# Kernel optimization log

Hardware: AMD Instinct MI355X
Metric: run time of the kernel (lower is better)

## Reference

```python
import jax, jax.numpy as jnp
import numpy as np

N = 100000
E = 1200000
D = 64
OUT_A = 2
OUT_B = 21


def setup_inputs() -> dict:
    key = jax.random.key(0)
    ks = jax.random.split(key, 12)
    v = jax.random.normal(ks[0], (N, D), dtype=jnp.float32)
    edge_src = jax.random.randint(ks[1], (E,), 0, N, dtype=jnp.int32)
    edge_dst = jax.random.randint(ks[2], (E,), 0, N, dtype=jnp.int32)
    rel_type = jax.random.randint(ks[3], (E,), 0, 3, dtype=jnp.int32)
    norm = jax.random.uniform(ks[4], (E,), dtype=jnp.float32)
    # relation weights per layer, kaiming-uniform-ish scale
    bound = float(np.sqrt(6.0 / D))
    W1 = jax.random.uniform(ks[5], (3, D, D), dtype=jnp.float32, minval=-bound, maxval=bound)
    W2 = jax.random.uniform(ks[6], (3, D, D), dtype=jnp.float32, minval=-bound, maxval=bound)
    W3 = jax.random.uniform(ks[7], (3, D, D), dtype=jnp.float32, minval=-bound, maxval=bound)
    Wa = jax.random.uniform(ks[8], (OUT_A, D), dtype=jnp.float32, minval=-bound, maxval=bound)
    ba = jnp.zeros((OUT_A,), dtype=jnp.float32)
    Wb = jax.random.uniform(ks[9], (OUT_B, D), dtype=jnp.float32, minval=-bound, maxval=bound)
    bb = jnp.zeros((OUT_B,), dtype=jnp.float32)
    return {"v": v, "edge_src": edge_src, "edge_dst": edge_dst, "rel_type": rel_type,
            "norm": norm, "W1": W1, "W2": W2, "W3": W3,
            "Wa": Wa, "ba": ba, "Wb": Wb, "bb": bb}


def _rgcn_layer(x, W, edge_src, edge_dst, rel_type, norm, skip):
    # Transform all nodes by each of the 3 relation matrices (cheap: 3 small GEMMs),
    # then gather per-edge: equivalent to bmm(h_src[e], W[rel_type[e]]).
    hr = jnp.einsum('nd,rde->rne', x, W)            # [3, N, D]
    msg = hr[rel_type, edge_src] * norm[:, None]     # [E, D]
    agg = jax.ops.segment_sum(msg, edge_dst, num_segments=x.shape[0])  # [N, D]
    return jax.nn.relu(agg + x) if skip else jax.nn.relu(agg)


def reference(v, edge_src, edge_dst, rel_type, norm, W1, W2, W3, Wa, ba, Wb, bb):
    x = _rgcn_layer(v, W1, edge_src, edge_dst, rel_type, norm, skip=False)
    x = _rgcn_layer(x, W2, edge_src, edge_dst, rel_type, norm, skip=True)
    x = _rgcn_layer(x, W3, edge_src, edge_dst, rel_type, norm, skip=True)
    xa = x @ Wa.T + ba
    xb = x @ Wb.T + bb
    return (xa, xb)
```

## Files before the change

kernel.cpp:

```cpp
#include <hip/hip_runtime.h>

#define D 64
#define NREL 3
#define SRC_MASK 0x1FFFF
#define ATHR 512
#define APT 8
#define ABLK (ATHR * APT)
#define BSH 9
#define BSZ 512

typedef unsigned short bf16_t;
typedef __attribute__((ext_vector_type(8))) short short8v;
typedef __attribute__((ext_vector_type(4))) float float4v;

__device__ __forceinline__ float bf2f(unsigned int u16) {
  return __uint_as_float(u16 << 16);
}
__device__ __forceinline__ unsigned int f2bf(float f) {
  unsigned int x = __float_as_uint(f);
  return (x + 0x7fffu + ((x >> 16) & 1u)) >> 16;
}

__global__ __launch_bounds__(512) void zero_kernel(int* __restrict__ a,
                                                   int* __restrict__ b, int n) {
  const int t = threadIdx.x;
  for (int i = t; i < n; i += 512) { a[i] = 0; b[i] = 0; }
}

__global__ __launch_bounds__(256) void conv_kernel(
    const float* __restrict__ in, bf16_t* __restrict__ out, int n4) {
  const int i = blockIdx.x * 256 + threadIdx.x;
  if (i >= n4) return;
  const float4 f = reinterpret_cast<const float4*>(in)[i];
  uint2 o;
  o.x = f2bf(f.x) | (f2bf(f.y) << 16);
  o.y = f2bf(f.z) | (f2bf(f.w) << 16);
  reinterpret_cast<uint2*>(out)[i] = o;
}

__global__ __launch_bounds__(256) void transform_kernel(
    const bf16_t* __restrict__ xb, const float* __restrict__ W,
    bf16_t* __restrict__ hr, int n_nodes) {
  __shared__ bf16_t wt[NREL * 64 * 72];
  const int tid = threadIdx.x;

  for (int idx = tid; idx < NREL * 64 * 64; idx += 256) {
    const int r = idx >> 12;
    const int k = (idx >> 6) & 63;
    const int od = idx & 63;
    wt[(r * 64 + od) * 72 + k] = (bf16_t)f2bf(W[idx]);
  }
  __syncthreads();

  const int wid = tid >> 6;
  const int lane = tid & 63;
  const int n0 = blockIdx.x * 64 + wid * 16;
  if (n0 >= n_nodes) return;

  const bf16_t* xrow = &xb[(long)(n0 + (lane & 15)) * 64 + (lane >> 4) * 8];
  const short8v bx0 = *reinterpret_cast<const short8v*>(xrow);
  const short8v bx1 = *reinterpret_cast<const short8v*>(xrow + 32);

  const int node = n0 + (lane & 15);
#pragma unroll
  for (int r = 0; r < NREL; ++r) {
#pragma unroll
    for (int t = 0; t < 4; ++t) {
      const bf16_t* wrow =
          &wt[(r * 64 + t * 16 + (lane & 15)) * 72 + (lane >> 4) * 8];
      const short8v a0 = *reinterpret_cast<const short8v*>(wrow);
      const short8v a1 = *reinterpret_cast<const short8v*>(wrow + 32);
      float4v acc = {0.f, 0.f, 0.f, 0.f};
      acc = __builtin_amdgcn_mfma_f32_16x16x32_bf16(a0, bx0, acc, 0, 0, 0);
      acc = __builtin_amdgcn_mfma_f32_16x16x32_bf16(a1, bx1, acc, 0, 0, 0);
      const int od = t * 16 + (lane >> 4) * 4;
      uint2 o;
      o.x = f2bf(acc[0]) | (f2bf(acc[1]) << 16);
      o.y = f2bf(acc[2]) | (f2bf(acc[3]) << 16);
      *reinterpret_cast<uint2*>(&hr[((long)r * n_nodes + node) * 64 + od]) = o;
    }
  }
}

__global__ __launch_bounds__(ATHR) void bhist_kernel(
    const int* __restrict__ dst, int* __restrict__ bdeg, int n_edges, int nb) {
  __shared__ int cnt[200];
  const int t = threadIdx.x;
  for (int b = t; b < nb; b += ATHR) cnt[b] = 0;
  __syncthreads();
  const long e0 = (long)blockIdx.x * ABLK;
#pragma unroll
  for (int i = 0; i < APT; ++i) {
    const long e = e0 + t + (long)i * ATHR;
    if (e < n_edges) atomicAdd(&cnt[dst[e] >> BSH], 1);
  }
  __syncthreads();
  for (int b = t; b < nb; b += ATHR)
    if (cnt[b]) atomicAdd(&bdeg[b], cnt[b]);
}

__global__ __launch_bounds__(512) void bscan_kernel(
    const int* __restrict__ bdeg, int* __restrict__ boffs, int nb) {
  __shared__ int s[512];
  const int t = threadIdx.x;
  const int v = (t < nb) ? bdeg[t] : 0;
  s[t] = v;
  __syncthreads();
  for (int off = 1; off < 512; off <<= 1) {
    const int add = (t >= off) ? s[t - off] : 0;
    __syncthreads();
    s[t] += add;
    __syncthreads();
  }
  if (t < nb) boffs[t] = s[t] - v;
  if (t == 511) boffs[nb] = s[nb - 1];
}

__global__ __launch_bounds__(ATHR) void binA_kernel(
    const int* __restrict__ src, const int* __restrict__ dst,
    const int* __restrict__ rel, const float* __restrict__ norm,
    const int* __restrict__ boffs, int* __restrict__ bcur,
    int2* __restrict__ binpay, int n_edges, int nb) {
  __shared__ int cnt[200];
  __shared__ int basea[200];
  const int t = threadIdx.x;
  const long e0 = (long)blockIdx.x * ABLK;

  for (int b = t; b < nb; b += ATHR) cnt[b] = 0;
  __syncthreads();

  int2 pay[APT];
  int bk[APT], slot[APT];
#pragma unroll
  for (int i = 0; i < APT; ++i) {
    const long e = e0 + t + (long)i * ATHR;
    if (e < n_edges) {
      const int d = dst[e];
      bk[i] = d >> BSH;
      pay[i] = make_int2(src[e] | (rel[e] << 17) | ((d & (BSZ - 1)) << 19),
                         __float_as_int(norm[e]));
      slot[i] = atomicAdd(&cnt[bk[i]], 1);
    } else {
      bk[i] = -1;
    }
  }
  __syncthreads();

  for (int b = t; b < nb; b += ATHR) {
    const int c = cnt[b];
    basea[b] = c ? (boffs[b] + atomicAdd(&bcur[b], c)) : 0;
  }
  __syncthreads();

#pragma unroll
  for (int i = 0; i < APT; ++i) {
    if (bk[i] >= 0) binpay[basea[bk[i]] + slot[i]] = pay[i];
  }
}

__global__ __launch_bounds__(512) void binB_kernel(
    const int2* __restrict__ binpay, const int* __restrict__ boffs,
    int2* __restrict__ edgebuf, int* __restrict__ deg, int* __restrict__ offs,
    int n_nodes) {
  __shared__ int cnt[512];
  __shared__ int ss[512];
  __shared__ int cur[512];
  const int b = blockIdx.x;
  const int t = threadIdx.x;
  cnt[t] = 0;
  __syncthreads();
  const int start = boffs[b];
  const int end = boffs[b + 1];
  for (int i = start + t; i < end; i += 512)
    atomicAdd(&cnt[((unsigned)binpay[i].x >> 19) & (BSZ - 1)], 1);
  __syncthreads();
  const int v = cnt[t];
  ss[t] = v;
  __syncthreads();
  for (int off = 1; off < 512; off <<= 1) {
    const int add = (t >= off) ? ss[t - off] : 0;
    __syncthreads();
    ss[t] += add;
    __syncthreads();
  }
  const int excl = ss[t] - v;
  cur[t] = excl;
  const int node = (b << BSH) + t;
  if (node < n_nodes) {
    deg[node] = v;
    offs[node] = start + excl;
  }
  __syncthreads();
  for (int i = start + t; i < end; i += 512) {
    const int2 pay = binpay[i];
    const int dl = ((unsigned)pay.x >> 19) & (BSZ - 1);
    const int pos = start + atomicAdd(&cur[dl], 1);
    edgebuf[pos] = pay;
  }
}

__global__ __launch_bounds__(256) void gather_kernel(
    const bf16_t* __restrict__ hr, const int2* __restrict__ edgebuf,
    const int* __restrict__ offs, const int* __restrict__ deg,
    const float* __restrict__ skip, float* __restrict__ out,
    bf16_t* __restrict__ xbout, int n_nodes) {
  const long gid = (long)blockIdx.x * 256 + threadIdx.x;
  const int n = (int)(gid >> 3);
  if (n >= n_nodes) return;
  const int c = (int)(gid & 7) * 8;

  const int beg = offs[n];
  const int cnt = deg[n];

  float acc0[8], acc1[8];
#pragma unroll
  for (int j = 0; j < 8; ++j) { acc0[j] = 0.f; acc1[j] = 0.f; }

  int i = 0;
  for (; i + 3 < cnt; i += 4) {
    const int2 e0 = edgebuf[beg + i];
    const int2 e1 = edgebuf[beg + i + 1];
    const int2 e2 = edgebuf[beg + i + 2];
    const int2 e3 = edgebuf[beg + i + 3];
    const uint4 v0 = *reinterpret_cast<const uint4*>(
        &hr[((long)((((unsigned)e0.x) >> 17) & 3) * n_nodes + (e0.x & SRC_MASK)) * 64 + c]);
    const uint4 v1 = *reinterpret_cast<const uint4*>(
        &hr[((long)((((unsigned)e1.x) >> 17) & 3) * n_nodes + (e1.x & SRC_MASK)) * 64 + c]);
    const uint4 v2 = *reinterpret_cast<const uint4*>(
        &hr[((long)((((unsigned)e2.x) >> 17) & 3) * n_nodes + (e2.x & SRC_MASK)) * 64 + c]);
    const uint4 v3 = *reinterpret_cast<const uint4*>(
        &hr[((long)((((unsigned)e3.x) >> 17) & 3) * n_nodes + (e3.x & SRC_MASK)) * 64 + c]);
    const float n0 = __int_as_float(e0.y), n1 = __int_as_float(e1.y);
    const float n2 = __int_as_float(e2.y), n3 = __int_as_float(e3.y);
    const unsigned int w0[4] = {v0.x, v0.y, v0.z, v0.w};
    const unsigned int w1[4] = {v1.x, v1.y, v1.z, v1.w};
    const unsigned int w2[4] = {v2.x, v2.y, v2.z, v2.w};
    const unsigned int w3[4] = {v3.x, v3.y, v3.z, v3.w};
#pragma unroll
    for (int j = 0; j < 4; ++j) {
      acc0[2 * j + 0] += bf2f(w0[j] & 0xffff) * n0;
      acc0[2 * j + 1] += bf2f(w0[j] >> 16) * n0;
      acc1[2 * j + 0] += bf2f(w1[j] & 0xffff) * n1;
      acc1[2 * j + 1] += bf2f(w1[j] >> 16) * n1;
      acc0[2 * j + 0] += bf2f(w2[j] & 0xffff) * n2;
      acc0[2 * j + 1] += bf2f(w2[j] >> 16) * n2;
      acc1[2 * j + 0] += bf2f(w3[j] & 0xffff) * n3;
      acc1[2 * j + 1] += bf2f(w3[j] >> 16) * n3;
    }
  }
  for (; i < cnt; ++i) {
    const int2 ea = edgebuf[beg + i];
    const float na = __int_as_float(ea.y);
    const uint4 va = *reinterpret_cast<const uint4*>(
        &hr[((long)((((unsigned)ea.x) >> 17) & 3) * n_nodes + (ea.x & SRC_MASK)) * 64 + c]);
    const unsigned int wa[4] = {va.x, va.y, va.z, va.w};
#pragma unroll
    for (int j = 0; j < 4; ++j) {
      acc0[2 * j + 0] += bf2f(wa[j] & 0xffff) * na;
      acc0[2 * j + 1] += bf2f(wa[j] >> 16) * na;
    }
  }

  float a[8];
#pragma unroll
  for (int j = 0; j < 8; ++j) a[j] = acc0[j] + acc1[j];
  if (skip != nullptr) {
    const float4 s0 = *reinterpret_cast<const float4*>(&skip[(long)n * 64 + c]);
    const float4 s1 = *reinterpret_cast<const float4*>(&skip[(long)n * 64 + c + 4]);
    a[0] += s0.x; a[1] += s0.y; a[2] += s0.z; a[3] += s0.w;
    a[4] += s1.x; a[5] += s1.y; a[6] += s1.z; a[7] += s1.w;
  }
#pragma unroll
  for (int j = 0; j < 8; ++j) a[j] = fmaxf(a[j], 0.f);
  float4 o0 = {a[0], a[1], a[2], a[3]};
  float4 o1 = {a[4], a[5], a[6], a[7]};
  *reinterpret_cast<float4*>(&out[(long)n * 64 + c]) = o0;
  *reinterpret_cast<float4*>(&out[(long)n * 64 + c + 4]) = o1;
  if (xbout != nullptr) {
    uint4 ob;
    ob.x = f2bf(a[0]) | (f2bf(a[1]) << 16);
    ob.y = f2bf(a[2]) | (f2bf(a[3]) << 16);
    ob.z = f2bf(a[4]) | (f2bf(a[5]) << 16);
    ob.w = f2bf(a[6]) | (f2bf(a[7]) << 16);
    *reinterpret_cast<uint4*>(&xbout[(long)n * 64 + c]) = ob;
  }
}

__global__ __launch_bounds__(256) void heads_kernel(
    const float* __restrict__ x, const float* __restrict__ Wa,
    const float* __restrict__ ba, const float* __restrict__ Wb,
    const float* __restrict__ bb, float* __restrict__ out, int n_nodes) {
  __shared__ float xs[64][65];
  __shared__ float wlt[64][24];
  __shared__ float bl[23];
  const int tid = threadIdx.x;
  const int base = blockIdx.x * 64;

  for (int idx = tid; idx < 2 * 64; idx += 256)
    wlt[idx & 63][idx >> 6] = Wa[idx];
  for (int idx = tid; idx < 21 * 64; idx += 256)
    wlt[idx & 63][2 + (idx >> 6)] = Wb[idx];
  if (tid < 2) bl[tid] = ba[tid];
  else if (tid < 23) bl[tid] = bb[tid - 2];
  const int nrows = min(64, n_nodes - base);
  for (int idx = tid; idx < nrows * 64; idx += 256)
    xs[idx >> 6][idx & 63] = x[(long)base * 64 + idx];
  __syncthreads();

  for (int idx = tid; idx < nrows * 23; idx += 256) {
    const int n = idx / 23;
    const int s = idx % 23;
    float acc = 0.f;
#pragma unroll
    for (int k = 0; k < 64; ++k) acc += xs[n][k] * wlt[k][s];
    acc += bl[s];
    const long node = base + n;
    if (s < 2) out[node * 2 + s] = acc;
    else out[(long)n_nodes * 2 + node * 21 + (s - 2)] = acc;
  }
}

static inline char* align_up(char* p, size_t a) {
  return (char*)(((uintptr_t)p + a - 1) & ~(uintptr_t)(a - 1));
}

extern "C" void kernel_launch(void* const* d_in, const int* in_sizes, int n_in,
                              void* d_out, int out_size, void* d_ws, size_t ws_size,
                              hipStream_t stream) {
  const float* v    = (const float*)d_in[0];
  const int*   esrc = (const int*)d_in[1];
  const int*   edst = (const int*)d_in[2];
  const int*   erel = (const int*)d_in[3];
  const float* norm = (const float*)d_in[4];
  const float* W1   = (const float*)d_in[5];
  const float* W2   = (const float*)d_in[6];
  const float* W3   = (const float*)d_in[7];
  const float* Wa   = (const float*)d_in[8];
  const float* ba   = (const float*)d_in[9];
  const float* Wb   = (const float*)d_in[10];
  const float* bb   = (const float*)d_in[11];

  const int nN = in_sizes[0] / D;
  const int E  = in_sizes[1];
  const int nb = (nN + BSZ - 1) >> BSH;

  char* p = (char*)d_ws;
  bf16_t* hr = (bf16_t*)p;            p += 3L * nN * D * sizeof(bf16_t);
  p = align_up(p, 16);
  bf16_t* xb = (bf16_t*)p;            p += (long)nN * D * sizeof(bf16_t);
  p = align_up(p, 16);
  float* bufA = (float*)p;            p += (long)nN * D * sizeof(float);
  float* bufB = (float*)p;            p += (long)nN * D * sizeof(float);
  int* deg      = (int*)p;            p += (long)nN * sizeof(int);
  int* offs     = (int*)p;            p += (long)nN * sizeof(int);
  int* bdeg     = (int*)p;            p += (long)nb * sizeof(int);
  int* boffs    = (int*)p;            p += (long)(nb + 1) * sizeof(int);
  int* bcur     = (int*)p;            p += (long)nb * sizeof(int);
  p = align_up(p, 16);
  int2* edgebuf = (int2*)p;           p += (long)E * sizeof(int2);
  int2* binpay  = (int2*)p;           p += (long)E * sizeof(int2);

  const int tblocks = (nN + 63) / 64;
  const int gblocks = (int)(((long)nN * 8 + 255) / 256);
  const int hblocks = (E + ABLK - 1) / ABLK;
  const int cblocks = (nN * D / 4 + 255) / 256;

  zero_kernel<<<1, 512, 0, stream>>>(bdeg, bcur, nb);
  bhist_kernel<<<hblocks, ATHR, 0, stream>>>(edst, bdeg, E, nb);
  bscan_kernel<<<1, 512, 0, stream>>>(bdeg, boffs, nb);
  binA_kernel<<<hblocks, ATHR, 0, stream>>>(esrc, edst, erel, norm, boffs, bcur,
                                            binpay, E, nb);
  binB_kernel<<<nb, 512, 0, stream>>>(binpay, boffs, edgebuf, deg, offs, nN);

  conv_kernel<<<cblocks, 256, 0, stream>>>(v, xb, nN * D / 4);
  transform_kernel<<<tblocks, 256, 0, stream>>>(xb, W1, hr, nN);
  gather_kernel<<<gblocks, 256, 0, stream>>>(hr, edgebuf, offs, deg, nullptr,
                                             bufA, xb, nN);

  transform_kernel<<<tblocks, 256, 0, stream>>>(xb, W2, hr, nN);
  gather_kernel<<<gblocks, 256, 0, stream>>>(hr, edgebuf, offs, deg, bufA,
                                             bufB, xb, nN);

  transform_kernel<<<tblocks, 256, 0, stream>>>(xb, W3, hr, nN);
  gather_kernel<<<gblocks, 256, 0, stream>>>(hr, edgebuf, offs, deg, bufB,
                                             bufA, nullptr, nN);

  heads_kernel<<<tblocks, 256, 0, stream>>>(bufA, Wa, ba, Wb, bb, (float*)d_out, nN);
}
```

Baseline: 262.5 us.

## Fuse fp32-to-bf16 conversion into transform and last gather into heads

The standalone conversion kernel is removed: the first transform now reads fp32 node features directly and converts them to bf16 in registers. The final gather layer is fused with the output heads, so relu'd node features are kept in shared memory and projected without writing and re-reading a full fp32 buffer. This cuts two kernel launches and several full-size passes over global memory, at the cost of a small duplicated weight load in each fused block and a sync that makes all 256 threads wait for the slowest gathering node.

```diff
diff --git a/kernel.cpp b/kernel.cpp
--- a/kernel.cpp
+++ b/kernel.cpp
@@ -27,19 +27,9 @@
   for (int i = t; i < n; i += 512) { a[i] = 0; b[i] = 0; }
 }
 
-__global__ __launch_bounds__(256) void conv_kernel(
-    const float* __restrict__ in, bf16_t* __restrict__ out, int n4) {
-  const int i = blockIdx.x * 256 + threadIdx.x;
-  if (i >= n4) return;
-  const float4 f = reinterpret_cast<const float4*>(in)[i];
-  uint2 o;
-  o.x = f2bf(f.x) | (f2bf(f.y) << 16);
-  o.y = f2bf(f.z) | (f2bf(f.w) << 16);
-  reinterpret_cast<uint2*>(out)[i] = o;
-}
-
+template <bool F32IN>
 __global__ __launch_bounds__(256) void transform_kernel(
-    const bf16_t* __restrict__ xb, const float* __restrict__ W,
+    const void* __restrict__ xin, const float* __restrict__ W,
     bf16_t* __restrict__ hr, int n_nodes) {
   __shared__ bf16_t wt[NREL * 64 * 72];
   const int tid = threadIdx.x;
@@ -57,9 +47,28 @@
   const int n0 = blockIdx.x * 64 + wid * 16;
   if (n0 >= n_nodes) return;
 
-  const bf16_t* xrow = &xb[(long)(n0 + (lane & 15)) * 64 + (lane >> 4) * 8];
-  const short8v bx0 = *reinterpret_cast<const short8v*>(xrow);
-  const short8v bx1 = *reinterpret_cast<const short8v*>(xrow + 32);
+  short8v bx0, bx1;
+  if constexpr (F32IN) {
+    const float* xrow =
+        (const float*)xin + (long)(n0 + (lane & 15)) * 64 + (lane >> 4) * 8;
+    const float4 f0 = *reinterpret_cast<const float4*>(xrow);
+    const float4 f1 = *reinterpret_cast<const float4*>(xrow + 4);
+    const float4 f2 = *reinterpret_cast<const float4*>(xrow + 32);
+    const float4 f3 = *reinterpret_cast<const float4*>(xrow + 36);
+    bx0[0] = (short)f2bf(f0.x); bx0[1] = (short)f2bf(f0.y);
+    bx0[2] = (short)f2bf(f0.z); bx0[3] = (short)f2bf(f0.w);
+    bx0[4] = (short)f2bf(f1.x); bx0[5] = (short)f2bf(f1.y);
+    bx0[6] = (short)f2bf(f1.z); bx0[7] = (short)f2bf(f1.w);
+    bx1[0] = (short)f2bf(f2.x); bx1[1] = (short)f2bf(f2.y);
+    bx1[2] = (short)f2bf(f2.z); bx1[3] = (short)f2bf(f2.w);
+    bx1[4] = (short)f2bf(f3.x); bx1[5] = (short)f2bf(f3.y);
+    bx1[6] = (short)f2bf(f3.z); bx1[7] = (short)f2bf(f3.w);
+  } else {
+    const bf16_t* xrow =
+        (const bf16_t*)xin + (long)(n0 + (lane & 15)) * 64 + (lane >> 4) * 8;
+    bx0 = *reinterpret_cast<const short8v*>(xrow);
+    bx1 = *reinterpret_cast<const short8v*>(xrow + 32);
+  }
 
   const int node = n0 + (lane & 15);
 #pragma unroll
@@ -199,19 +208,9 @@
   }
 }
 
-__global__ __launch_bounds__(256) void gather_kernel(
+__device__ __forceinline__ void gather_core(
     const bf16_t* __restrict__ hr, const int2* __restrict__ edgebuf,
-    const int* __restrict__ offs, const int* __restrict__ deg,
-    const float* __restrict__ skip, float* __restrict__ out,
-    bf16_t* __restrict__ xbout, int n_nodes) {
-  const long gid = (long)blockIdx.x * 256 + threadIdx.x;
-  const int n = (int)(gid >> 3);
-  if (n >= n_nodes) return;
-  const int c = (int)(gid & 7) * 8;
-
-  const int beg = offs[n];
-  const int cnt = deg[n];
-
+    int beg, int cnt, int n_nodes, int c, float* a ) {
   float acc0[8], acc1[8];
 #pragma unroll
   for (int j = 0; j < 8; ++j) { acc0[j] = 0.f; acc1[j] = 0.f; }
@@ -260,10 +259,22 @@
       acc0[2 * j + 1] += bf2f(wa[j] >> 16) * na;
     }
   }
+#pragma unroll
+  for (int j = 0; j < 8; ++j) a[j] = acc0[j] + acc1[j];
+}
+
+__global__ __launch_bounds__(256) void gather_kernel(
+    const bf16_t* __restrict__ hr, const int2* __restrict__ edgebuf,
+    const int* __restrict__ offs, const int* __restrict__ deg,
+    const float* __restrict__ skip, float* __restrict__ out,
+    bf16_t* __restrict__ xbout, int n_nodes) {
+  const long gid = (long)blockIdx.x * 256 + threadIdx.x;
+  const int n = (int)(gid >> 3);
+  if (n >= n_nodes) return;
+  const int c = (int)(gid & 7) * 8;
 
   float a[8];
-#pragma unroll
-  for (int j = 0; j < 8; ++j) a[j] = acc0[j] + acc1[j];
+  gather_core(hr, edgebuf, offs[n], deg[n], n_nodes, c, a);
   if (skip != nullptr) {
     const float4 s0 = *reinterpret_cast<const float4*>(&skip[(long)n * 64 + c]);
     const float4 s1 = *reinterpret_cast<const float4*>(&skip[(long)n * 64 + c + 4]);
@@ -276,45 +287,63 @@
   float4 o1 = {a[4], a[5], a[6], a[7]};
   *reinterpret_cast<float4*>(&out[(long)n * 64 + c]) = o0;
   *reinterpret_cast<float4*>(&out[(long)n * 64 + c + 4]) = o1;
-  if (xbout != nullptr) {
-    uint4 ob;
-    ob.x = f2bf(a[0]) | (f2bf(a[1]) << 16);
-    ob.y = f2bf(a[2]) | (f2bf(a[3]) << 16);
-    ob.z = f2bf(a[4]) | (f2bf(a[5]) << 16);
-    ob.w = f2bf(a[6]) | (f2bf(a[7]) << 16);
-    *reinterpret_cast<uint4*>(&xbout[(long)n * 64 + c]) = ob;
-  }
-}
-
-__global__ __launch_bounds__(256) void heads_kernel(
-    const float* __restrict__ x, const float* __restrict__ Wa,
+  uint4 ob;
+  ob.x = f2bf(a[0]) | (f2bf(a[1]) << 16);
+  ob.y = f2bf(a[2]) | (f2bf(a[3]) << 16);
+  ob.z = f2bf(a[4]) | (f2bf(a[5]) << 16);
+  ob.w = f2bf(a[6]) | (f2bf(a[7]) << 16);
+  *reinterpret_cast<uint4*>(&xbout[(long)n * 64 + c]) = ob;
+}
+
+__global__ __launch_bounds__(256) void gather_heads_kernel(
+    const bf16_t* __restrict__ hr, const int2* __restrict__ edgebuf,
+    const int* __restrict__ offs, const int* __restrict__ deg,
+    const float* __restrict__ skip, const float* __restrict__ Wa,
     const float* __restrict__ ba, const float* __restrict__ Wb,
     const float* __restrict__ bb, float* __restrict__ out, int n_nodes) {
-  __shared__ float xs[64][65];
+  __shared__ float xs[32][72];
   __shared__ float wlt[64][24];
   __shared__ float bl[23];
   const int tid = threadIdx.x;
-  const int base = blockIdx.x * 64;
-
-  for (int idx = tid; idx < 2 * 64; idx += 256)
-    wlt[idx & 63][idx >> 6] = Wa[idx];
+
+  for (int idx = tid; idx < 2 * 64; idx += 256) wlt[idx & 63][idx >> 6] = Wa[idx];
   for (int idx = tid; idx < 21 * 64; idx += 256)
     wlt[idx & 63][2 + (idx >> 6)] = Wb[idx];
   if (tid < 2) bl[tid] = ba[tid];
   else if (tid < 23) bl[tid] = bb[tid - 2];
-  const int nrows = min(64, n_nodes - base);
-  for (int idx = tid; idx < nrows * 64; idx += 256)
-    xs[idx >> 6][idx & 63] = x[(long)base * 64 + idx];
-  __syncthreads();
-
+
+  const int nbase = blockIdx.x * 32;
+  const int nl = tid >> 3;
+  const int n = nbase + nl;
+  const int c = (tid & 7) * 8;
+
+  if (n < n_nodes) {
+    float a[8];
+    gather_core(hr, edgebuf, offs[n], deg[n], n_nodes, c, a);
+    if (skip != nullptr) {
+      const float4 s0 = *reinterpret_cast<const float4*>(&skip[(long)n * 64 + c]);
+      const float4 s1 = *reinterpret_cast<const float4*>(&skip[(long)n * 64 + c + 4]);
+      a[0] += s0.x; a[1] += s0.y; a[2] += s0.z; a[3] += s0.w;
+      a[4] += s1.x; a[5] += s1.y; a[6] += s1.z; a[7] += s1.w;
+    }
+#pragma unroll
+    for (int j = 0; j < 8; ++j) a[j] = fmaxf(a[j], 0.f);
+    float4 o0 = {a[0], a[1], a[2], a[3]};
+    float4 o1 = {a[4], a[5], a[6], a[7]};
+    *reinterpret_cast<float4*>(&xs[nl][c]) = o0;
+    *reinterpret_cast<float4*>(&xs[nl][c + 4]) = o1;
+  }
+  __syncthreads();
+
+  const int nrows = min(32, n_nodes - nbase);
   for (int idx = tid; idx < nrows * 23; idx += 256) {
-    const int n = idx / 23;
+    const int nn = idx / 23;
     const int s = idx % 23;
     float acc = 0.f;
 #pragma unroll
-    for (int k = 0; k < 64; ++k) acc += xs[n][k] * wlt[k][s];
+    for (int k = 0; k < 64; ++k) acc += xs[nn][k] * wlt[k][s];
     acc += bl[s];
-    const long node = base + n;
+    const long node = nbase + nn;
     if (s < 2) out[node * 2 + s] = acc;
     else out[(long)n_nodes * 2 + node * 21 + (s - 2)] = acc;
   }
@@ -362,8 +391,8 @@
 
   const int tblocks = (nN + 63) / 64;
   const int gblocks = (int)(((long)nN * 8 + 255) / 256);
+  const int ghblocks = (nN + 31) / 32;
   const int hblocks = (E + ABLK - 1) / ABLK;
-  const int cblocks = (nN * D / 4 + 255) / 256;
 
   zero_kernel<<<1, 512, 0, stream>>>(bdeg, bcur, nb);
   bhist_kernel<<<hblocks, ATHR, 0, stream>>>(edst, bdeg, E, nb);
@@ -372,18 +401,16 @@
                                             binpay, E, nb);
   binB_kernel<<<nb, 512, 0, stream>>>(binpay, boffs, edgebuf, deg, offs, nN);
 
-  conv_kernel<<<cblocks, 256, 0, stream>>>(v, xb, nN * D / 4);
-  transform_kernel<<<tblocks, 256, 0, stream>>>(xb, W1, hr, nN);
+  transform_kernel<true><<<tblocks, 256, 0, stream>>>(v, W1, hr, nN);
   gather_kernel<<<gblocks, 256, 0, stream>>>(hr, edgebuf, offs, deg, nullptr,
                                              bufA, xb, nN);
 
-  transform_kernel<<<tblocks, 256, 0, stream>>>(xb, W2, hr, nN);
+  transform_kernel<false><<<tblocks, 256, 0, stream>>>(xb, W2, hr, nN);
   gather_kernel<<<gblocks, 256, 0, stream>>>(hr, edgebuf, offs, deg, bufA,
                                              bufB, xb, nN);
 
-  transform_kernel<<<tblocks, 256, 0, stream>>>(xb, W3, hr, nN);
-  gather_kernel<<<gblocks, 256, 0, stream>>>(hr, edgebuf, offs, deg, bufB,
-                                             bufA, nullptr, nN);
-
-  heads_kernel<<<tblocks, 256, 0, stream>>>(bufA, Wa, ba, Wb, bb, (float*)d_out, nN);
-}
+  transform_kernel<false><<<tblocks, 256, 0, stream>>>(xb, W3, hr, nN);
+  gather_heads_kernel<<<ghblocks, 256, 0, stream>>>(hr, edgebuf, offs, deg, bufB,
+                                                    Wa, ba, Wb, bb,
+                                                    (float*)d_out, nN);
+}
```

Result: faster. 236.7 us (-9.8%).

## Aggregate raw features per relation before the weight transform, fuse last layer with heads

Applied to the files above, without the earlier changes.

Each layer now gathers bf16 node features from a single N×64 table into three per-relation accumulators, then applies the relation weights with MFMA afterward (aggregate-then-transform). This replaces gathering from a three times larger transformed table. Skip connections and intermediates stay in bf16 instead of fp32, and the last layer's mixing is fused with the output heads. The edge binning pass now stages payloads in shared memory so the global writes are contiguous. In exchange, the per-relation aggregates are rounded to bf16 before the GEMM, and each gather thread holds three accumulator sets, which adds register pressure.

```diff
diff --git a/kernel.cpp b/kernel.cpp
--- a/kernel.cpp
+++ b/kernel.cpp
@@ -38,50 +38,6 @@
   reinterpret_cast<uint2*>(out)[i] = o;
 }
 
-__global__ __launch_bounds__(256) void transform_kernel(
-    const bf16_t* __restrict__ xb, const float* __restrict__ W,
-    bf16_t* __restrict__ hr, int n_nodes) {
-  __shared__ bf16_t wt[NREL * 64 * 72];
-  const int tid = threadIdx.x;
-
-  for (int idx = tid; idx < NREL * 64 * 64; idx += 256) {
-    const int r = idx >> 12;
-    const int k = (idx >> 6) & 63;
-    const int od = idx & 63;
-    wt[(r * 64 + od) * 72 + k] = (bf16_t)f2bf(W[idx]);
-  }
-  __syncthreads();
-
-  const int wid = tid >> 6;
-  const int lane = tid & 63;
-  const int n0 = blockIdx.x * 64 + wid * 16;
-  if (n0 >= n_nodes) return;
-
-  const bf16_t* xrow = &xb[(long)(n0 + (lane & 15)) * 64 + (lane >> 4) * 8];
-  const short8v bx0 = *reinterpret_cast<const short8v*>(xrow);
-  const short8v bx1 = *reinterpret_cast<const short8v*>(xrow + 32);
-
-  const int node = n0 + (lane & 15);
-#pragma unroll
-  for (int r = 0; r < NREL; ++r) {
-#pragma unroll
-    for (int t = 0; t < 4; ++t) {
-      const bf16_t* wrow =
-          &wt[(r * 64 + t * 16 + (lane & 15)) * 72 + (lane >> 4) * 8];
-      const short8v a0 = *reinterpret_cast<const short8v*>(wrow);
-      const short8v a1 = *reinterpret_cast<const short8v*>(wrow + 32);
-      float4v acc = {0.f, 0.f, 0.f, 0.f};
-      acc = __builtin_amdgcn_mfma_f32_16x16x32_bf16(a0, bx0, acc, 0, 0, 0);
-      acc = __builtin_amdgcn_mfma_f32_16x16x32_bf16(a1, bx1, acc, 0, 0, 0);
-      const int od = t * 16 + (lane >> 4) * 4;
-      uint2 o;
-      o.x = f2bf(acc[0]) | (f2bf(acc[1]) << 16);
-      o.y = f2bf(acc[2]) | (f2bf(acc[3]) << 16);
-      *reinterpret_cast<uint2*>(&hr[((long)r * n_nodes + node) * 64 + od]) = o;
-    }
-  }
-}
-
 __global__ __launch_bounds__(ATHR) void bhist_kernel(
     const int* __restrict__ dst, int* __restrict__ bdeg, int n_edges, int nb) {
   __shared__ int cnt[200];
@@ -121,12 +77,15 @@
     const int* __restrict__ rel, const float* __restrict__ norm,
     const int* __restrict__ boffs, int* __restrict__ bcur,
     int2* __restrict__ binpay, int n_edges, int nb) {
-  __shared__ int cnt[200];
-  __shared__ int basea[200];
+  __shared__ int cnt[256];
+  __shared__ int incl[256];
+  __shared__ int gbase[200];
+  __shared__ int2 staged[ABLK];
+  __shared__ unsigned char sbk[ABLK];
   const int t = threadIdx.x;
   const long e0 = (long)blockIdx.x * ABLK;
 
-  for (int b = t; b < nb; b += ATHR) cnt[b] = 0;
+  for (int b = t; b < 256; b += ATHR) cnt[b] = 0;
   __syncthreads();
 
   int2 pay[APT];
@@ -146,15 +105,37 @@
   }
   __syncthreads();
 
+  if (t < 256) incl[t] = cnt[t];
+  __syncthreads();
+  for (int off = 1; off < 256; off <<= 1) {
+    int add = 0;
+    if (t < 256 && t >= off) add = incl[t - off];
+    __syncthreads();
+    if (t < 256) incl[t] += add;
+    __syncthreads();
+  }
+
   for (int b = t; b < nb; b += ATHR) {
     const int c = cnt[b];
-    basea[b] = c ? (boffs[b] + atomicAdd(&bcur[b], c)) : 0;
+    gbase[b] = c ? (boffs[b] + atomicAdd(&bcur[b], c)) : 0;
   }
   __syncthreads();
 
 #pragma unroll
   for (int i = 0; i < APT; ++i) {
-    if (bk[i] >= 0) binpay[basea[bk[i]] + slot[i]] = pay[i];
+    if (bk[i] >= 0) {
+      const int pos = incl[bk[i]] - cnt[bk[i]] + slot[i];
+      staged[pos] = pay[i];
+      sbk[pos] = (unsigned char)bk[i];
+    }
+  }
+  __syncthreads();
+
+  const int nv = (int)min((long)ABLK, (long)(n_edges - e0));
+  for (int j = t; j < nv; j += ATHR) {
+    const int b = sbk[j];
+    const int excl = incl[b] - cnt[b];
+    binpay[gbase[b] + j - excl] = staged[j];
   }
 }
 
@@ -199,11 +180,32 @@
   }
 }
 
-__global__ __launch_bounds__(256) void gather_kernel(
-    const bf16_t* __restrict__ hr, const int2* __restrict__ edgebuf,
+#define ACC_EDGE(V, NF, RR)                                               \
+  do {                                                                    \
+    const unsigned ww0 = V.x, ww1 = V.y, ww2 = V.z, ww3 = V.w;            \
+    const float nf_ = NF;                                                 \
+    if (RR == 0) {                                                        \
+      a0[0] += bf2f(ww0 & 0xffff) * nf_; a0[1] += bf2f(ww0 >> 16) * nf_;  \
+      a0[2] += bf2f(ww1 & 0xffff) * nf_; a0[3] += bf2f(ww1 >> 16) * nf_;  \
+      a0[4] += bf2f(ww2 & 0xffff) * nf_; a0[5] += bf2f(ww2 >> 16) * nf_;  \
+      a0[6] += bf2f(ww3 & 0xffff) * nf_; a0[7] += bf2f(ww3 >> 16) * nf_;  \
+    } else if (RR == 1) {                                                 \
+      a1[0] += bf2f(ww0 & 0xffff) * nf_; a1[1] += bf2f(ww0 >> 16) * nf_;  \
+      a1[2] += bf2f(ww1 & 0xffff) * nf_; a1[3] += bf2f(ww1 >> 16) * nf_;  \
+      a1[4] += bf2f(ww2 & 0xffff) * nf_; a1[5] += bf2f(ww2 >> 16) * nf_;  \
+      a1[6] += bf2f(ww3 & 0xffff) * nf_; a1[7] += bf2f(ww3 >> 16) * nf_;  \
+    } else {                                                              \
+      a2[0] += bf2f(ww0 & 0xffff) * nf_; a2[1] += bf2f(ww0 >> 16) * nf_;  \
+      a2[2] += bf2f(ww1 & 0xffff) * nf_; a2[3] += bf2f(ww1 >> 16) * nf_;  \
+      a2[4] += bf2f(ww2 & 0xffff) * nf_; a2[5] += bf2f(ww2 >> 16) * nf_;  \
+      a2[6] += bf2f(ww3 & 0xffff) * nf_; a2[7] += bf2f(ww3 >> 16) * nf_;  \
+    }                                                                     \
+  } while (0)
+
+__global__ __launch_bounds__(256) void gather_agg_kernel(
+    const bf16_t* __restrict__ xb, const int2* __restrict__ edgebuf,
     const int* __restrict__ offs, const int* __restrict__ deg,
-    const float* __restrict__ skip, float* __restrict__ out,
-    bf16_t* __restrict__ xbout, int n_nodes) {
+    bf16_t* __restrict__ agg, int n_nodes) {
   const long gid = (long)blockIdx.x * 256 + threadIdx.x;
   const int n = (int)(gid >> 3);
   if (n >= n_nodes) return;
@@ -212,9 +214,9 @@
   const int beg = offs[n];
   const int cnt = deg[n];
 
-  float acc0[8], acc1[8];
-#pragma unroll
-  for (int j = 0; j < 8; ++j) { acc0[j] = 0.f; acc1[j] = 0.f; }
+  float a0[8], a1[8], a2[8];
+#pragma unroll
+  for (int j = 0; j < 8; ++j) { a0[j] = 0.f; a1[j] = 0.f; a2[j] = 0.f; }
 
   int i = 0;
   for (; i + 3 < cnt; i += 4) {
@@ -222,101 +224,172 @@
     const int2 e1 = edgebuf[beg + i + 1];
     const int2 e2 = edgebuf[beg + i + 2];
     const int2 e3 = edgebuf[beg + i + 3];
-    const uint4 v0 = *reinterpret_cast<const uint4*>(
-        &hr[((long)((((unsigned)e0.x) >> 17) & 3) * n_nodes + (e0.x & SRC_MASK)) * 64 + c]);
-    const uint4 v1 = *reinterpret_cast<const uint4*>(
-        &hr[((long)((((unsigned)e1.x) >> 17) & 3) * n_nodes + (e1.x & SRC_MASK)) * 64 + c]);
-    const uint4 v2 = *reinterpret_cast<const uint4*>(
-        &hr[((long)((((unsigned)e2.x) >> 17) & 3) * n_nodes + (e2.x & SRC_MASK)) * 64 + c]);
-    const uint4 v3 = *reinterpret_cast<const uint4*>(
-        &hr[((long)((((unsigned)e3.x) >> 17) & 3) * n_nodes + (e3.x & SRC_MASK)) * 64 + c]);
-    const float n0 = __int_as_float(e0.y), n1 = __int_as_float(e1.y);
-    const float n2 = __int_as_float(e2.y), n3 = __int_as_float(e3.y);
-    const unsigned int w0[4] = {v0.x, v0.y, v0.z, v0.w};
-    const unsigned int w1[4] = {v1.x, v1.y, v1.z, v1.w};
-    const unsigned int w2[4] = {v2.x, v2.y, v2.z, v2.w};
-    const unsigned int w3[4] = {v3.x, v3.y, v3.z, v3.w};
-#pragma unroll
-    for (int j = 0; j < 4; ++j) {
-      acc0[2 * j + 0] += bf2f(w0[j] & 0xffff) * n0;
-      acc0[2 * j + 1] += bf2f(w0[j] >> 16) * n0;
-      acc1[2 * j + 0] += bf2f(w1[j] & 0xffff) * n1;
-      acc1[2 * j + 1] += bf2f(w1[j] >> 16) * n1;
-      acc0[2 * j + 0] += bf2f(w2[j] & 0xffff) * n2;
-      acc0[2 * j + 1] += bf2f(w2[j] >> 16) * n2;
-      acc1[2 * j + 0] += bf2f(w3[j] & 0xffff) * n3;
-      acc1[2 * j + 1] += bf2f(w3[j] >> 16) * n3;
-    }
+    const uint4 v0 = *reinterpret_cast<const uint4*>(&xb[(long)(e0.x & SRC_MASK) * 64 + c]);
+    const uint4 v1 = *reinterpret_cast<const uint4*>(&xb[(long)(e1.x & SRC_MASK) * 64 + c]);
+    const uint4 v2 = *reinterpret_cast<const uint4*>(&xb[(long)(e2.x & SRC_MASK) * 64 + c]);
+    const uint4 v3 = *reinterpret_cast<const uint4*>(&xb[(long)(e3.x & SRC_MASK) * 64 + c]);
+    const int r0 = (e0.x >> 17) & 3, r1 = (e1.x >> 17) & 3;
+    const int r2 = (e2.x >> 17) & 3, r3 = (e3.x >> 17) & 3;
+    ACC_EDGE(v0, __int_as_float(e0.y), r0);
+    ACC_EDGE(v1, __int_as_float(e1.y), r1);
+    ACC_EDGE(v2, __int_as_float(e2.y), r2);
+    ACC_EDGE(v3, __int_as_float(e3.y), r3);
   }
   for (; i < cnt; ++i) {
     const int2 ea = edgebuf[beg + i];
-    const float na = __int_as_float(ea.y);
-    const uint4 va = *reinterpret_cast<const uint4*>(
-        &hr[((long)((((unsigned)ea.x) >> 17) & 3) * n_nodes + (ea.x & SRC_MASK)) * 64 + c]);
-    const unsigned int wa[4] = {va.x, va.y, va.z, va.w};
-#pragma unroll
-    for (int j = 0; j < 4; ++j) {
-      acc0[2 * j + 0] += bf2f(wa[j] & 0xffff) * na;
-      acc0[2 * j + 1] += bf2f(wa[j] >> 16) * na;
-    }
-  }
-
-  float a[8];
-#pragma unroll
-  for (int j = 0; j < 8; ++j) a[j] = acc0[j] + acc1[j];
-  if (skip != nullptr) {
-    const float4 s0 = *reinterpret_cast<const float4*>(&skip[(long)n * 64 + c]);
-    const float4 s1 = *reinterpret_cast<const float4*>(&skip[(long)n * 64 + c + 4]);
-    a[0] += s0.x; a[1] += s0.y; a[2] += s0.z; a[3] += s0.w;
-    a[4] += s1.x; a[5] += s1.y; a[6] += s1.z; a[7] += s1.w;
-  }
-#pragma unroll
-  for (int j = 0; j < 8; ++j) a[j] = fmaxf(a[j], 0.f);
-  float4 o0 = {a[0], a[1], a[2], a[3]};
-  float4 o1 = {a[4], a[5], a[6], a[7]};
-  *reinterpret_cast<float4*>(&out[(long)n * 64 + c]) = o0;
-  *reinterpret_cast<float4*>(&out[(long)n * 64 + c + 4]) = o1;
-  if (xbout != nullptr) {
-    uint4 ob;
-    ob.x = f2bf(a[0]) | (f2bf(a[1]) << 16);
-    ob.y = f2bf(a[2]) | (f2bf(a[3]) << 16);
-    ob.z = f2bf(a[4]) | (f2bf(a[5]) << 16);
-    ob.w = f2bf(a[6]) | (f2bf(a[7]) << 16);
-    *reinterpret_cast<uint4*>(&xbout[(long)n * 64 + c]) = ob;
-  }
-}
-
-__global__ __launch_bounds__(256) void heads_kernel(
-    const float* __restrict__ x, const float* __restrict__ Wa,
+    const uint4 va = *reinterpret_cast<const uint4*>(&xb[(long)(ea.x & SRC_MASK) * 64 + c]);
+    const int ra = (ea.x >> 17) & 3;
+    ACC_EDGE(va, __int_as_float(ea.y), ra);
+  }
+
+  uint4 o;
+  o.x = f2bf(a0[0]) | (f2bf(a0[1]) << 16);
+  o.y = f2bf(a0[2]) | (f2bf(a0[3]) << 16);
+  o.z = f2bf(a0[4]) | (f2bf(a0[5]) << 16);
+  o.w = f2bf(a0[6]) | (f2bf(a0[7]) << 16);
+  *reinterpret_cast<uint4*>(&agg[((long)0 * n_nodes + n) * 64 + c]) = o;
+  o.x = f2bf(a1[0]) | (f2bf(a1[1]) << 16);
+  o.y = f2bf(a1[2]) | (f2bf(a1[3]) << 16);
+  o.z = f2bf(a1[4]) | (f2bf(a1[5]) << 16);
+  o.w = f2bf(a1[6]) | (f2bf(a1[7]) << 16);
+  *reinterpret_cast<uint4*>(&agg[((long)1 * n_nodes + n) * 64 + c]) = o;
+  o.x = f2bf(a2[0]) | (f2bf(a2[1]) << 16);
+  o.y = f2bf(a2[2]) | (f2bf(a2[3]) << 16);
+  o.z = f2bf(a2[4]) | (f2bf(a2[5]) << 16);
+  o.w = f2bf(a2[6]) | (f2bf(a2[7]) << 16);
+  *reinterpret_cast<uint4*>(&agg[((long)2 * n_nodes + n) * 64 + c]) = o;
+}
+
+template <bool SKIP>
+__global__ __launch_bounds__(256) void mix_kernel(
+    const bf16_t* __restrict__ agg, const float* __restrict__ W,
+    const bf16_t* __restrict__ skip, bf16_t* __restrict__ xbout, int n_nodes) {
+  __shared__ bf16_t wt[NREL * 64 * 72];
+  const int tid = threadIdx.x;
+
+  for (int idx = tid; idx < NREL * 64 * 64; idx += 256) {
+    const int r = idx >> 12;
+    const int k = (idx >> 6) & 63;
+    const int od = idx & 63;
+    wt[(r * 64 + od) * 72 + k] = (bf16_t)f2bf(W[idx]);
+  }
+  __syncthreads();
+
+  const int wid = tid >> 6;
+  const int lane = tid & 63;
+  const int n0 = blockIdx.x * 64 + wid * 16;
+  if (n0 >= n_nodes) return;
+  const int node = n0 + (lane & 15);
+
+  short8v bx[NREL][2];
+#pragma unroll
+  for (int r = 0; r < NREL; ++r) {
+    const bf16_t* arow = &agg[((long)r * n_nodes + node) * 64 + (lane >> 4) * 8];
+    bx[r][0] = *reinterpret_cast<const short8v*>(arow);
+    bx[r][1] = *reinterpret_cast<const short8v*>(arow + 32);
+  }
+
+#pragma unroll
+  for (int t = 0; t < 4; ++t) {
+    float4v acc = {0.f, 0.f, 0.f, 0.f};
+#pragma unroll
+    for (int r = 0; r < NREL; ++r) {
+      const bf16_t* wrow = &wt[(r * 64 + t * 16 + (lane & 15)) * 72 + (lane >> 4) * 8];
+      const short8v w0 = *reinterpret_cast<const short8v*>(wrow);
+      const short8v w1 = *reinterpret_cast<const short8v*>(wrow + 32);
+      acc = __builtin_amdgcn_mfma_f32_16x16x32_bf16(w0, bx[r][0], acc, 0, 0, 0);
+      acc = __builtin_amdgcn_mfma_f32_16x16x32_bf16(w1, bx[r][1], acc, 0, 0, 0);
+    }
+    const int od = t * 16 + (lane >> 4) * 4;
+    float vals[4] = {acc[0], acc[1], acc[2], acc[3]};
+    if constexpr (SKIP) {
+      const uint2 s = *reinterpret_cast<const uint2*>(&skip[(long)node * 64 + od]);
+      vals[0] += bf2f(s.x & 0xffff);
+      vals[1] += bf2f(s.x >> 16);
+      vals[2] += bf2f(s.y & 0xffff);
+      vals[3] += bf2f(s.y >> 16);
+    }
+#pragma unroll
+    for (int j = 0; j < 4; ++j) vals[j] = fmaxf(vals[j], 0.f);
+    uint2 o;
+    o.x = f2bf(vals[0]) | (f2bf(vals[1]) << 16);
+    o.y = f2bf(vals[2]) | (f2bf(vals[3]) << 16);
+    *reinterpret_cast<uint2*>(&xbout[(long)node * 64 + od]) = o;
+  }
+}
+
+__global__ __launch_bounds__(256) void mix_heads_kernel(
+    const bf16_t* __restrict__ agg, const float* __restrict__ W,
+    const bf16_t* __restrict__ skip, const float* __restrict__ Wa,
     const float* __restrict__ ba, const float* __restrict__ Wb,
     const float* __restrict__ bb, float* __restrict__ out, int n_nodes) {
-  __shared__ float xs[64][65];
+  __shared__ bf16_t wt[NREL * 64 * 72];
+  __shared__ float xs[64][72];
   __shared__ float wlt[64][24];
   __shared__ float bl[23];
   const int tid = threadIdx.x;
-  const int base = blockIdx.x * 64;
-
-  for (int idx = tid; idx < 2 * 64; idx += 256)
-    wlt[idx & 63][idx >> 6] = Wa[idx];
+
+  for (int idx = tid; idx < NREL * 64 * 64; idx += 256) {
+    const int r = idx >> 12;
+    const int k = (idx >> 6) & 63;
+    const int od = idx & 63;
+    wt[(r * 64 + od) * 72 + k] = (bf16_t)f2bf(W[idx]);
+  }
+  for (int idx = tid; idx < 2 * 64; idx += 256) wlt[idx & 63][idx >> 6] = Wa[idx];
   for (int idx = tid; idx < 21 * 64; idx += 256)
     wlt[idx & 63][2 + (idx >> 6)] = Wb[idx];
   if (tid < 2) bl[tid] = ba[tid];
   else if (tid < 23) bl[tid] = bb[tid - 2];
-  const int nrows = min(64, n_nodes - base);
-  for (int idx = tid; idx < nrows * 64; idx += 256)
-    xs[idx >> 6][idx & 63] = x[(long)base * 64 + idx];
-  __syncthreads();
-
+  __syncthreads();
+
+  const int wid = tid >> 6;
+  const int lane = tid & 63;
+  const int n0 = blockIdx.x * 64 + wid * 16;
+  const bool active = (n0 < n_nodes);
+  const int node = n0 + (lane & 15);
+
+  if (active) {
+    short8v bx[NREL][2];
+#pragma unroll
+    for (int r = 0; r < NREL; ++r) {
+      const bf16_t* arow = &agg[((long)r * n_nodes + node) * 64 + (lane >> 4) * 8];
+      bx[r][0] = *reinterpret_cast<const short8v*>(arow);
+      bx[r][1] = *reinterpret_cast<const short8v*>(arow + 32);
+    }
+#pragma unroll
+    for (int t = 0; t < 4; ++t) {
+      float4v acc = {0.f, 0.f, 0.f, 0.f};
+#pragma unroll
+      for (int r = 0; r < NREL; ++r) {
+        const bf16_t* wrow = &wt[(r * 64 + t * 16 + (lane & 15)) * 72 + (lane >> 4) * 8];
+        const short8v w0 = *reinterpret_cast<const short8v*>(wrow);
+        const short8v w1 = *reinterpret_cast<const short8v*>(wrow + 32);
+        acc = __builtin_amdgcn_mfma_f32_16x16x32_bf16(w0, bx[r][0], acc, 0, 0, 0);
+        acc = __builtin_amdgcn_mfma_f32_16x16x32_bf16(w1, bx[r][1], acc, 0, 0, 0);
+      }
+      const int od = t * 16 + (lane >> 4) * 4;
+      const uint2 s = *reinterpret_cast<const uint2*>(&skip[(long)node * 64 + od]);
+      const int nl = wid * 16 + (lane & 15);
+      xs[nl][od + 0] = fmaxf(acc[0] + bf2f(s.x & 0xffff), 0.f);
+      xs[nl][od + 1] = fmaxf(acc[1] + bf2f(s.x >> 16), 0.f);
+      xs[nl][od + 2] = fmaxf(acc[2] + bf2f(s.y & 0xffff), 0.f);
+      xs[nl][od + 3] = fmaxf(acc[3] + bf2f(s.y >> 16), 0.f);
+    }
+  }
+  __syncthreads();
+
+  const int nbase = blockIdx.x * 64;
+  const int nrows = min(64, n_nodes - nbase);
   for (int idx = tid; idx < nrows * 23; idx += 256) {
-    const int n = idx / 23;
-    const int s = idx % 23;
+    const int nn = idx / 23;
+    const int sjj = idx % 23;
     float acc = 0.f;
 #pragma unroll
-    for (int k = 0; k < 64; ++k) acc += xs[n][k] * wlt[k][s];
-    acc += bl[s];
-    const long node = base + n;
-    if (s < 2) out[node * 2 + s] = acc;
-    else out[(long)n_nodes * 2 + node * 21 + (s - 2)] = acc;
+    for (int k = 0; k < 64; ++k) acc += xs[nn][k] * wlt[k][sjj];
+    acc += bl[sjj];
+    const long gnode = nbase + nn;
+    if (sjj < 2) out[gnode * 2 + sjj] = acc;
+    else out[(long)n_nodes * 2 + gnode * 21 + (sjj - 2)] = acc;
   }
 }
 
@@ -345,12 +418,12 @@
   const int nb = (nN + BSZ - 1) >> BSH;
 
   char* p = (char*)d_ws;
-  bf16_t* hr = (bf16_t*)p;            p += 3L * nN * D * sizeof(bf16_t);
+  bf16_t* agg = (bf16_t*)p;           p += 3L * nN * D * sizeof(bf16_t);
   p = align_up(p, 16);
-  bf16_t* xb = (bf16_t*)p;            p += (long)nN * D * sizeof(bf16_t);
+  bf16_t* xbA = (bf16_t*)p;           p += (long)nN * D * sizeof(bf16_t);
   p = align_up(p, 16);
-  float* bufA = (float*)p;            p += (long)nN * D * sizeof(float);
-  float* bufB = (float*)p;            p += (long)nN * D * sizeof(float);
+  bf16_t* xbB = (bf16_t*)p;           p += (long)nN * D * sizeof(bf16_t);
+  p = align_up(p, 16);
   int* deg      = (int*)p;            p += (long)nN * sizeof(int);
   int* offs     = (int*)p;            p += (long)nN * sizeof(int);
   int* bdeg     = (int*)p;            p += (long)nb * sizeof(int);
@@ -372,18 +445,14 @@
                                             binpay, E, nb);
   binB_kernel<<<nb, 512, 0, stream>>>(binpay, boffs, edgebuf, deg, offs, nN);
 
-  conv_kernel<<<cblocks, 256, 0, stream>>>(v, xb, nN * D / 4);
-  transform_kernel<<<tblocks, 256, 0, stream>>>(xb, W1, hr, nN);
-  gather_kernel<<<gblocks, 256, 0, stream>>>(hr, edgebuf, offs, deg, nullptr,
-                                             bufA, xb, nN);
-
-  transform_kernel<<<tblocks, 256, 0, stream>>>(xb, W2, hr, nN);
-  gather_kernel<<<gblocks, 256, 0, stream>>>(hr, edgebuf, offs, deg, bufA,
-                                             bufB, xb, nN);
-
-  transform_kernel<<<tblocks, 256, 0, stream>>>(xb, W3, hr, nN);
-  gather_kernel<<<gblocks, 256, 0, stream>>>(hr, edgebuf, offs, deg, bufB,
-                                             bufA, nullptr, nN);
-
-  heads_kernel<<<tblocks, 256, 0, stream>>>(bufA, Wa, ba, Wb, bb, (float*)d_out, nN);
-}
+  conv_kernel<<<cblocks, 256, 0, stream>>>(v, xbA, nN * D / 4);
+  gather_agg_kernel<<<gblocks, 256, 0, stream>>>(xbA, edgebuf, offs, deg, agg, nN);
+  mix_kernel<false><<<tblocks, 256, 0, stream>>>(agg, W1, nullptr, xbB, nN);
+
+  gather_agg_kernel<<<gblocks, 256, 0, stream>>>(xbB, edgebuf, offs, deg, agg, nN);
+  mix_kernel<true><<<tblocks, 256, 0, stream>>>(agg, W2, xbB, xbA, nN);
+
+  gather_agg_kernel<<<gblocks, 256, 0, stream>>>(xbA, edgebuf, offs, deg, agg, nN);
+  mix_heads_kernel<<<tblocks, 256, 0, stream>>>(agg, W3, xbA, Wa, ba, Wb, bb,
+                                                (float*)d_out, nN);
+}
```

After: 236.7 us. 9.8% less time.
